# Kernel tuning notes

Measured on AMD Instinct MI355X. Metric: run time of the kernel, lower is better.

Reference implementation:

```python
import jax, jax.numpy as jnp
import numpy as np

SUB_NO = 20
T_NO = 201
E_NO = 2000
I_NO = 500
T_DATA = 20000

def _make_cden():
    C = np.zeros((SUB_NO, SUB_NO), dtype=np.float32)
    for i in range(SUB_NO):
        for c in (2 * i + 1, 2 * i + 2):
            if c < SUB_NO:
                C[i, c] = 1.0
    return C

C_DEN = _make_cden()
CHILDREN = [np.where(C_DEN[s] == 1)[0] for s in range(SUB_NO)]  # static tree structure


def setup_inputs() -> dict:
    key = jax.random.key(0)
    ks = jax.random.split(key, 12)
    eps = 1e-6
    inp = {}
    inp['S_e'] = jax.random.uniform(ks[0], (T_DATA, E_NO), dtype=jnp.float32)
    inp['S_i'] = jax.random.uniform(ks[1], (T_DATA, I_NO), dtype=jnp.float32)
    # uniform noise for REBAR reparam; clipped away from {0,1} so log(-log(u)) is finite
    inp['u'] = jnp.clip(jax.random.uniform(ks[2], (SUB_NO, E_NO + I_NO), dtype=jnp.float32), eps, 1.0 - eps)
    inp['v'] = jnp.clip(jax.random.uniform(ks[3], (SUB_NO, E_NO + I_NO), dtype=jnp.float32), eps, 1.0 - eps)
    inp['W_syn'] = jax.random.normal(ks[4], (SUB_NO, 2), dtype=jnp.float32) * 0.1
    inp['Tau_syn'] = jnp.ones((SUB_NO, 2), dtype=jnp.float32)
    inp['Delta_syn'] = jax.random.uniform(ks[5], (SUB_NO, 2), dtype=jnp.float32)
    inp['W_sub'] = jax.random.uniform(ks[6], (SUB_NO,), dtype=jnp.float32)
    inp['V_o'] = jax.random.normal(ks[7], (1,), dtype=jnp.float32)
    inp['Theta'] = jnp.zeros((SUB_NO,), dtype=jnp.float32)
    inp['C_syn_log'] = jnp.ones((SUB_NO, E_NO + I_NO), dtype=jnp.float32)
    return inp


def _H(x):
    # one-hot of per-column argmax (first max, as torch.argmax)
    idx = jnp.argmax(x, axis=0)
    return jax.nn.one_hot(idx, x.shape[0], axis=0, dtype=x.dtype)


def _reparam_pz(u, theta):
    return jnp.log(theta) - jnp.log(-jnp.log(u))


def _reparam_pz_b(v, b, theta):
    # b is one-hot per column; v_k = v at the b==1 row of each column
    v_k = jnp.sum(v * b, axis=0, keepdims=True)  # [1, cols]
    z_same = -jnp.log(-jnp.log(v))
    z_diff = -jnp.log(-jnp.log(v) / theta - jnp.log(v_k))
    return b * z_same + (1.0 - b) * z_diff


def _evaluate_f(C_syn, S_e, S_i, W_syn, Tau_syn, Delta_syn, W_sub, V_o):
    T_data = S_e.shape[0]
    C_syn_e = C_syn[:, :E_NO]          # [sub, E]
    C_syn_i = C_syn[:, -I_NO:]         # [sub, I]
    # double-exponential (alpha) synaptic kernels, vectorized over subunits & e/i
    t_raw = jnp.arange(T_NO, dtype=S_e.dtype)                               # [T_no]
    t = jnp.maximum(t_raw[None, None, :] - jnp.exp(Delta_syn)[:, :, None], 0.0)  # [sub,2,T_no]
    t_tau = t / jnp.exp(Tau_syn)[:, :, None]
    kern = t_tau * jnp.exp(-t_tau) * W_syn[:, :, None]                      # [sub,2,T_no]
    # project spikes onto subunits
    in_e = S_e @ C_syn_e.T   # [T, sub]
    in_i = S_i @ C_syn_i.T   # [T, sub]
    # causal depthwise conv: syn[t,s] = sum_tau kern[s,:,tau] * in[t-tau,s]
    inp = jnp.stack([in_e.T, in_i.T], axis=1).reshape(1, SUB_NO * 2, T_data)   # NCH
    k = jnp.flip(kern, axis=-1).reshape(SUB_NO * 2, 1, T_NO)                   # OIH
    filt = jax.lax.conv_general_dilated(
        inp, k, window_strides=(1,), padding=[(T_NO - 1, 0)],
        feature_group_count=SUB_NO * 2,
        dimension_numbers=('NCH', 'OIH', 'NCH'))
    syn_in = filt.reshape(SUB_NO, 2, T_data).sum(axis=1).T   # [T, sub]
    # tree-recurrent tanh aggregation (children have higher index than parents)
    sub_out = [None] * SUB_NO
    for s in range(SUB_NO):
        idx = SUB_NO - 1 - s
        ch = CHILDREN[idx]
        if ch.size == 0:
            sub_out[idx] = jnp.tanh(syn_in[:, idx])
        else:
            leaf = sum(sub_out[c] * W_sub[c] for c in ch)
            sub_out[idx] = jnp.tanh(syn_in[:, idx] + leaf)
    return sub_out[0] * W_sub[0] + V_o[0]


def reference(S_e, S_i, u, v, W_syn, Tau_syn, Delta_syn, W_sub, V_o, Theta, C_syn_log):
    theta = jax.nn.softmax(C_syn_log, axis=0)
    rebar_z = _reparam_pz(u, theta)
    hard_z = _H(rebar_z)
    rebar_zb = _reparam_pz_b(v, hard_z, theta)
    soft_z = jax.nn.sigmoid(rebar_z / 0.5) + 1e-9
    soft_zb = jax.nn.sigmoid(rebar_zb / 0.5) + 1e-9
    V_hard_z = _evaluate_f(hard_z, S_e, S_i, W_syn, Tau_syn, Delta_syn, W_sub, V_o)
    V_soft_z = _evaluate_f(soft_z, S_e, S_i, W_syn, Tau_syn, Delta_syn, W_sub, V_o)
    V_soft_zb = _evaluate_f(soft_zb, S_e, S_i, W_syn, Tau_syn, Delta_syn, W_sub, V_o)
    return (V_hard_z, V_soft_z, V_soft_zb, theta, hard_z, soft_z, soft_zb)
```

## Files before the change

### kernel.cpp

```cpp
#include <hip/hip_runtime.h>
#include <math.h>

#define SUBS 20
#define TAPS 201
#define ENO 2000
#define INO 500
#define TDATA 20000

typedef __bf16 bf16x8 __attribute__((ext_vector_type(8)));
typedef float f32x4 __attribute__((ext_vector_type(4)));

#define WGE_STRIDE 2048
#define WGI_STRIDE 512

#define WGE_OFF  0ull
#define WGI_OFF  262144ull
#define KERN_OFF 327680ull
#define INE_OFF  360448ull
#define INI_OFF  (INE_OFF + 4800000ull)
#define SYN_OFF  (INI_OFF + 4800000ull)

__device__ __forceinline__ unsigned short f2bf(float f) {
  union { float f; unsigned int u; } c; c.f = f;
  unsigned int u = c.u;
  return (unsigned short)((u + 0x7FFFu + ((u >> 16) & 1u)) >> 16);
}

__global__ __launch_bounds__(256) void prep_kernel(
    const float* __restrict__ u, const float* __restrict__ v,
    const float* __restrict__ C_log, const float* __restrict__ W_syn,
    const float* __restrict__ Tau_syn, const float* __restrict__ Delta_syn,
    float* __restrict__ out,
    unsigned short* __restrict__ wge, unsigned short* __restrict__ wgi,
    float* __restrict__ kern)
{
  if (blockIdx.x < 10) {
    const int n = blockIdx.x * 256 + threadIdx.x;
    if (n >= 2500) return;
    float x[SUBS], theta[SUBS], rebar[SUBS];
    float mx = -1e30f;
#pragma unroll
    for (int s = 0; s < SUBS; ++s) { x[s] = C_log[s*2500 + n]; mx = fmaxf(mx, x[s]); }
    float sum = 0.f;
#pragma unroll
    for (int s = 0; s < SUBS; ++s) { theta[s] = expf(x[s] - mx); sum += theta[s]; }
    const float inv = 1.f / sum;
    int idx = 0; float best = -1e30f;
#pragma unroll
    for (int s = 0; s < SUBS; ++s) {
      theta[s] *= inv;
      out[60000 + s*2500 + n] = theta[s];
      const float uu = u[s*2500 + n];
      const float r = logf(theta[s]) - logf(-logf(uu));
      rebar[s] = r;
      if (r > best) { best = r; idx = s; }
    }
    const float lvk = logf(v[idx*2500 + n]);
#pragma unroll
    for (int s = 0; s < SUBS; ++s) {
      const float hz = (s == idx) ? 1.f : 0.f;
      const float sz = 1.f / (1.f + expf(-2.f * rebar[s])) + 1e-9f;
      const float vv = v[s*2500 + n];
      const float zb = (s == idx) ? (-logf(-logf(vv)))
                                  : (-logf(-logf(vv) / theta[s] - lvk));
      const float szb = 1.f / (1.f + expf(-2.f * zb)) + 1e-9f;
      out[110000 + s*2500 + n] = hz;
      out[160000 + s*2500 + n] = sz;
      out[210000 + s*2500 + n] = szb;
      if (n < ENO) {
        wge[(s     )*WGE_STRIDE + n] = f2bf(hz);
        wge[(20 + s)*WGE_STRIDE + n] = f2bf(sz);
        wge[(40 + s)*WGE_STRIDE + n] = f2bf(szb);
      } else {
        const int k = n - ENO;
        wgi[(s     )*WGI_STRIDE + k] = f2bf(hz);
        wgi[(20 + s)*WGI_STRIDE + k] = f2bf(sz);
        wgi[(40 + s)*WGI_STRIDE + k] = f2bf(szb);
      }
    }
  } else {
    const int tid = threadIdx.x;
    for (int i = tid; i < 40*TAPS; i += 256) {
      const int ch = i / TAPS, m = i - ch*TAPS;
      const float dl  = expf(Delta_syn[ch]);
      const float tau = expf(Tau_syn[ch]);
      const float t  = fmaxf((float)m - dl, 0.f);
      const float tt = t / tau;
      kern[i] = tt * expf(-tt) * W_syn[ch];
    }
    for (int i = tid; i < 4*2048; i += 256) wge[(60 + (i >> 11))*WGE_STRIDE + (i & 2047)] = 0;
    for (int i = tid; i < 60*48;  i += 256) wge[(i / 48)*WGE_STRIDE + 2000 + (i % 48)] = 0;
    for (int i = tid; i < 4*512;  i += 256) wgi[(60 + (i >> 9))*WGI_STRIDE + (i & 511)] = 0;
    for (int i = tid; i < 60*12;  i += 256) wgi[(i / 12)*WGI_STRIDE + 500 + (i % 12)] = 0;
  }
}

__global__ __launch_bounds__(256) void gemm_kernel(
    const float* __restrict__ S_e, const float* __restrict__ S_i,
    const unsigned short* __restrict__ wge, const unsigned short* __restrict__ wgi,
    float* __restrict__ in_e, float* __restrict__ in_i, float* __restrict__ part)
{
  __shared__ unsigned short Alds[64*40];
  __shared__ unsigned short Blds[64*40];
  const int tid  = threadIdx.x;
  const int t0   = blockIdx.x * 64;
  const int chunk = blockIdx.y;
  const bool isE = (chunk < 2);
  const int wave = tid >> 6;
  const int lane = tid & 63;
  const int m16  = lane & 15;
  const int quad = lane >> 4;
  const int slotA = tid & 7;
  const int rowA  = tid >> 3;
  const int cB    = tid >> 2;
  const int slotB = tid & 3;

  const float* S = isE ? S_e : S_i;
  const unsigned short* Wg = isE ? wge : wgi;
  float* outp = (chunk == 0) ? in_e : ((chunk == 1) ? part : in_i);
  const int K       = isE ? ENO : INO;
  const int Wstride = isE ? WGE_STRIDE : WGI_STRIDE;
  const int k_base  = (chunk == 1) ? 1024 : 0;
  const int steps   = (chunk == 0) ? 32 : ((chunk == 1) ? 31 : 16);

  f32x4 acc0 = {0.f,0.f,0.f,0.f};
  f32x4 acc1 = acc0, acc2 = acc0, acc3 = acc0;

  for (int st = 0; st < steps; ++st) {
    const int k0 = k_base + st * 32;
#pragma unroll
    for (int p = 0; p < 2; ++p) {
      const int r = rowA + p*32;
      const int t = t0 + r;
      const int k = k0 + slotA*4;
      float4 val = make_float4(0.f, 0.f, 0.f, 0.f);
      if (t < TDATA) {
        if (k + 4 <= K) {
          val = *(const float4*)(S + (size_t)t*K + k);
        } else {
          val.x = (k+0 < K) ? S[(size_t)t*K + k+0] : 0.f;
          val.y = (k+1 < K) ? S[(size_t)t*K + k+1] : 0.f;
          val.z = (k+2 < K) ? S[(size_t)t*K + k+2] : 0.f;
          val.w = (k+3 < K) ? S[(size_t)t*K + k+3] : 0.f;
        }
      }
      ushort4 w4;
      w4.x = f2bf(val.x); w4.y = f2bf(val.y);
      w4.z = f2bf(val.z); w4.w = f2bf(val.w);
      *(ushort4*)(&Alds[r*40 + slotA*4]) = w4;
    }
    *(uint4*)(&Blds[cB*40 + slotB*8]) =
        *(const uint4*)(Wg + (size_t)cB*Wstride + k0 + slotB*8);
    __syncthreads();
    const bf16x8 a  = *(const bf16x8*)(&Alds[(wave*16 + m16)*40 + quad*8]);
    const bf16x8 b0 = *(const bf16x8*)(&Blds[(      m16)*40 + quad*8]);
    const bf16x8 b1 = *(const bf16x8*)(&Blds[(16 + m16)*40 + quad*8]);
    const bf16x8 b2 = *(const bf16x8*)(&Blds[(32 + m16)*40 + quad*8]);
    const bf16x8 b3 = *(const bf16x8*)(&Blds[(48 + m16)*40 + quad*8]);
    acc0 = __builtin_amdgcn_mfma_f32_16x16x32_bf16(a, b0, acc0, 0, 0, 0);
    acc1 = __builtin_amdgcn_mfma_f32_16x16x32_bf16(a, b1, acc1, 0, 0, 0);
    acc2 = __builtin_amdgcn_mfma_f32_16x16x32_bf16(a, b2, acc2, 0, 0, 0);
    acc3 = __builtin_amdgcn_mfma_f32_16x16x32_bf16(a, b3, acc3, 0, 0, 0);
    __syncthreads();
  }
  const int t = t0 + wave*16 + quad*4;
  if (t < TDATA) {
    float* o = outp + t;
    *(float4*)(o + (size_t)(     m16)*TDATA) = *(float4*)&acc0;
    *(float4*)(o + (size_t)(16 + m16)*TDATA) = *(float4*)&acc1;
    *(float4*)(o + (size_t)(32 + m16)*TDATA) = *(float4*)&acc2;
    if (m16 < 12)
      *(float4*)(o + (size_t)(48 + m16)*TDATA) = *(float4*)&acc3;
  }
}

__global__ __launch_bounds__(256) void reduce_kernel(
    float* __restrict__ in_e, const float* __restrict__ part)
{
  const int i = blockIdx.x * 256 + threadIdx.x;
  const int n4 = 60 * TDATA / 4;
  if (i < n4) {
    float4 a = ((const float4*)in_e)[i];
    const float4 p = ((const float4*)part)[i];
    a.x += p.x; a.y += p.y; a.z += p.z; a.w += p.w;
    ((float4*)in_e)[i] = a;
  }
}

__device__ __forceinline__ int swz(int i) { return i + (i >> 5); }

__global__ __launch_bounds__(256) void conv_kernel(
    const float* __restrict__ in_e, const float* __restrict__ in_i,
    const float* __restrict__ kern, float* __restrict__ syn)
{
  __shared__ float Ee[2320];
  __shared__ float Ei[2320];
  const int ch = blockIdx.y;
  const int t0 = blockIdx.x * 2048;
  const int s  = ch % SUBS;
  const float* pe = in_e + (size_t)ch * TDATA;
  const float* pi = in_i + (size_t)ch * TDATA;
  for (int i = threadIdx.x; i < 2248; i += 256) {
    const int g = t0 - 200 + i;
    const bool ok = (g >= 0) && (g < TDATA);
    Ee[swz(i)] = ok ? pe[g] : 0.f;
    Ei[swz(i)] = ok ? pi[g] : 0.f;
  }
  __syncthreads();
  const float* ke = kern + (size_t)(s*2    ) * TAPS;
  const float* ki = kern + (size_t)(s*2 + 1) * TAPS;
  const int tb = threadIdx.x * 8;
  float acc[8] = {0.f,0.f,0.f,0.f,0.f,0.f,0.f,0.f};
  float we[8], wi[8];
#pragma unroll
  for (int j = 0; j < 8; ++j) {
    we[j] = Ee[swz(tb + 200 + j)];
    wi[j] = Ei[swz(tb + 200 + j)];
  }
#pragma unroll 8
  for (int m = 0; m < TAPS; ++m) {
    const float k0 = ke[m];
    const float k1 = ki[m];
#pragma unroll
    for (int j = 0; j < 8; ++j)
      acc[j] = fmaf(we[j], k0, fmaf(wi[j], k1, acc[j]));
    if (m < TAPS - 1) {
#pragma unroll
      for (int j = 7; j > 0; --j) { we[j] = we[j-1]; wi[j] = wi[j-1]; }
      we[0] = Ee[swz(tb + 199 - m)];
      wi[0] = Ei[swz(tb + 199 - m)];
    }
  }
  const int t = t0 + tb;
  if (t < TDATA) {
    float* o = syn + (size_t)ch * TDATA + t;
    *(float4*)(o    ) = make_float4(acc[0], acc[1], acc[2], acc[3]);
    *(float4*)(o + 4) = make_float4(acc[4], acc[5], acc[6], acc[7]);
  }
}

__global__ __launch_bounds__(256) void tree_kernel(
    const float* __restrict__ syn, const float* __restrict__ W_sub,
    const float* __restrict__ V_o, float* __restrict__ out)
{
  const int t = blockIdx.x * 256 + threadIdx.x;
  const int var = blockIdx.y;
  if (t >= TDATA) return;
  const float* sp = syn + (size_t)var * SUBS * TDATA + t;
  float so[SUBS];
#pragma unroll
  for (int s = SUBS - 1; s >= 0; --s) {
    float val = sp[(size_t)s * TDATA];
    const int c1 = 2*s + 1, c2 = 2*s + 2;
    if (c1 < SUBS) val += so[c1] * W_sub[c1];
    if (c2 < SUBS) val += so[c2] * W_sub[c2];
    so[s] = tanhf(val);
  }
  out[(size_t)var * TDATA + t] = so[0] * W_sub[0] + V_o[0];
}

extern "C" void kernel_launch(void* const* d_in, const int* in_sizes, int n_in,
                              void* d_out, int out_size, void* d_ws, size_t ws_size,
                              hipStream_t stream) {
  const float* S_e     = (const float*)d_in[0];
  const float* S_i     = (const float*)d_in[1];
  const float* u       = (const float*)d_in[2];
  const float* v       = (const float*)d_in[3];
  const float* W_syn   = (const float*)d_in[4];
  const float* Tau_syn = (const float*)d_in[5];
  const float* Delta   = (const float*)d_in[6];
  const float* W_sub   = (const float*)d_in[7];
  const float* V_o     = (const float*)d_in[8];
  const float* C_log   = (const float*)d_in[10];
  float* out = (float*)d_out;
  char* ws = (char*)d_ws;
  unsigned short* wge = (unsigned short*)(ws + WGE_OFF);
  unsigned short* wgi = (unsigned short*)(ws + WGI_OFF);
  float* kern = (float*)(ws + KERN_OFF);
  float* in_e = (float*)(ws + INE_OFF);
  float* in_i = (float*)(ws + INI_OFF);
  float* syn  = (float*)(ws + SYN_OFF);

  prep_kernel<<<dim3(11), dim3(256), 0, stream>>>(u, v, C_log, W_syn, Tau_syn,
                                                  Delta, out, wge, wgi, kern);
  gemm_kernel<<<dim3(313, 3), dim3(256), 0, stream>>>(S_e, S_i, wge, wgi,
                                                      in_e, in_i, syn);
  reduce_kernel<<<dim3(1172), dim3(256), 0, stream>>>(in_e, syn);
  conv_kernel<<<dim3(10, 60), dim3(256), 0, stream>>>(in_e, in_i, kern, syn);
  tree_kernel<<<dim3(79, 3), dim3(256), 0, stream>>>(syn, W_sub, V_o, out);
}
```

Baseline: 343.6 us.

## Load GEMM operands straight to registers with prefetch and drop split-K reduce

The GEMM no longer stages operands in LDS. Each wave loads its own 16 rows of S and the bf16 weight fragments directly into registers, converts A to bf16 in registers, and prefetches the next K step while the current MFMAs run, so there are no block barriers. The split of the excitatory K range across two blocks, and the separate reduce kernel that summed the partial outputs, are removed. This saves a launch and a full read-modify-write pass over the 60x20000 intermediate. The costs are half as many blocks for the excitatory GEMM, which lowers parallelism on the bandwidth-bound S_e read, and redundant per-wave B loads served from cache. Tail reads are clamped to in-bounds addresses, and the zero-padded weights cancel the duplicated values.

Result: slower. 398.1 us (+15.9%).

```diff
diff --git a/kernel.cpp b/kernel.cpp
--- a/kernel.cpp
+++ b/kernel.cpp
@@ -9,6 +9,7 @@
 
 typedef __bf16 bf16x8 __attribute__((ext_vector_type(8)));
 typedef float f32x4 __attribute__((ext_vector_type(4)));
+typedef unsigned short ushort8 __attribute__((ext_vector_type(8)));
 
 #define WGE_STRIDE 2048
 #define WGI_STRIDE 512
@@ -98,93 +99,74 @@
 __global__ __launch_bounds__(256) void gemm_kernel(
     const float* __restrict__ S_e, const float* __restrict__ S_i,
     const unsigned short* __restrict__ wge, const unsigned short* __restrict__ wgi,
-    float* __restrict__ in_e, float* __restrict__ in_i, float* __restrict__ part)
-{
-  __shared__ unsigned short Alds[64*40];
-  __shared__ unsigned short Blds[64*40];
+    float* __restrict__ in_e, float* __restrict__ in_i)
+{
   const int tid  = threadIdx.x;
-  const int t0   = blockIdx.x * 64;
-  const int chunk = blockIdx.y;
-  const bool isE = (chunk < 2);
   const int wave = tid >> 6;
   const int lane = tid & 63;
   const int m16  = lane & 15;
   const int quad = lane >> 4;
-  const int slotA = tid & 7;
-  const int rowA  = tid >> 3;
-  const int cB    = tid >> 2;
-  const int slotB = tid & 3;
-
+  const int kq   = quad * 8;
+  const int t0   = blockIdx.x * 64 + wave * 16;
+  if (t0 >= TDATA) return;
+
+  const bool isE = (blockIdx.y == 0);
   const float* S = isE ? S_e : S_i;
   const unsigned short* Wg = isE ? wge : wgi;
-  float* outp = (chunk == 0) ? in_e : ((chunk == 1) ? part : in_i);
+  float* outp = isE ? in_e : in_i;
   const int K       = isE ? ENO : INO;
   const int Wstride = isE ? WGE_STRIDE : WGI_STRIDE;
-  const int k_base  = (chunk == 1) ? 1024 : 0;
-  const int steps   = (chunk == 0) ? 32 : ((chunk == 1) ? 31 : 16);
+  const int steps   = isE ? 63 : 16;
+
+  const float* Arow = S + (size_t)(t0 + m16) * K;
+  const unsigned short* Bp0 = Wg + (size_t)(     m16) * Wstride + kq;
+  const unsigned short* Bp1 = Wg + (size_t)(16 + m16) * Wstride + kq;
+  const unsigned short* Bp2 = Wg + (size_t)(32 + m16) * Wstride + kq;
+  const unsigned short* Bp3 = Wg + (size_t)(48 + m16) * Wstride + kq;
 
   f32x4 acc0 = {0.f,0.f,0.f,0.f};
   f32x4 acc1 = acc0, acc2 = acc0, acc3 = acc0;
 
+  auto ldA = [&](int k0, float4& lo, float4& hi) {
+    const int kb  = k0 + kq;
+    const int blo = (kb + 4 <= K) ? kb     : K - 4;
+    const int bhi = (kb + 8 <= K) ? kb + 4 : K - 4;
+    lo = *(const float4*)(Arow + blo);
+    hi = *(const float4*)(Arow + bhi);
+  };
+
+  float4 alo, ahi;
+  uint4 b0, b1, b2, b3;
+  ldA(0, alo, ahi);
+  b0 = *(const uint4*)(Bp0); b1 = *(const uint4*)(Bp1);
+  b2 = *(const uint4*)(Bp2); b3 = *(const uint4*)(Bp3);
+
   for (int st = 0; st < steps; ++st) {
-    const int k0 = k_base + st * 32;
-#pragma unroll
-    for (int p = 0; p < 2; ++p) {
-      const int r = rowA + p*32;
-      const int t = t0 + r;
-      const int k = k0 + slotA*4;
-      float4 val = make_float4(0.f, 0.f, 0.f, 0.f);
-      if (t < TDATA) {
-        if (k + 4 <= K) {
-          val = *(const float4*)(S + (size_t)t*K + k);
-        } else {
-          val.x = (k+0 < K) ? S[(size_t)t*K + k+0] : 0.f;
-          val.y = (k+1 < K) ? S[(size_t)t*K + k+1] : 0.f;
-          val.z = (k+2 < K) ? S[(size_t)t*K + k+2] : 0.f;
-          val.w = (k+3 < K) ? S[(size_t)t*K + k+3] : 0.f;
-        }
-      }
-      ushort4 w4;
-      w4.x = f2bf(val.x); w4.y = f2bf(val.y);
-      w4.z = f2bf(val.z); w4.w = f2bf(val.w);
-      *(ushort4*)(&Alds[r*40 + slotA*4]) = w4;
-    }
-    *(uint4*)(&Blds[cB*40 + slotB*8]) =
-        *(const uint4*)(Wg + (size_t)cB*Wstride + k0 + slotB*8);
-    __syncthreads();
-    const bf16x8 a  = *(const bf16x8*)(&Alds[(wave*16 + m16)*40 + quad*8]);
-    const bf16x8 b0 = *(const bf16x8*)(&Blds[(      m16)*40 + quad*8]);
-    const bf16x8 b1 = *(const bf16x8*)(&Blds[(16 + m16)*40 + quad*8]);
-    const bf16x8 b2 = *(const bf16x8*)(&Blds[(32 + m16)*40 + quad*8]);
-    const bf16x8 b3 = *(const bf16x8*)(&Blds[(48 + m16)*40 + quad*8]);
-    acc0 = __builtin_amdgcn_mfma_f32_16x16x32_bf16(a, b0, acc0, 0, 0, 0);
-    acc1 = __builtin_amdgcn_mfma_f32_16x16x32_bf16(a, b1, acc1, 0, 0, 0);
-    acc2 = __builtin_amdgcn_mfma_f32_16x16x32_bf16(a, b2, acc2, 0, 0, 0);
-    acc3 = __builtin_amdgcn_mfma_f32_16x16x32_bf16(a, b3, acc3, 0, 0, 0);
-    __syncthreads();
-  }
-  const int t = t0 + wave*16 + quad*4;
-  if (t < TDATA) {
-    float* o = outp + t;
-    *(float4*)(o + (size_t)(     m16)*TDATA) = *(float4*)&acc0;
-    *(float4*)(o + (size_t)(16 + m16)*TDATA) = *(float4*)&acc1;
-    *(float4*)(o + (size_t)(32 + m16)*TDATA) = *(float4*)&acc2;
-    if (m16 < 12)
-      *(float4*)(o + (size_t)(48 + m16)*TDATA) = *(float4*)&acc3;
-  }
-}
-
-__global__ __launch_bounds__(256) void reduce_kernel(
-    float* __restrict__ in_e, const float* __restrict__ part)
-{
-  const int i = blockIdx.x * 256 + threadIdx.x;
-  const int n4 = 60 * TDATA / 4;
-  if (i < n4) {
-    float4 a = ((const float4*)in_e)[i];
-    const float4 p = ((const float4*)part)[i];
-    a.x += p.x; a.y += p.y; a.z += p.z; a.w += p.w;
-    ((float4*)in_e)[i] = a;
-  }
+    const int kn = (st + 1 < steps) ? (st + 1) * 32 : st * 32;
+    float4 nalo, nahi;
+    ldA(kn, nalo, nahi);
+    const uint4 nb0 = *(const uint4*)(Bp0 + kn);
+    const uint4 nb1 = *(const uint4*)(Bp1 + kn);
+    const uint4 nb2 = *(const uint4*)(Bp2 + kn);
+    const uint4 nb3 = *(const uint4*)(Bp3 + kn);
+
+    ushort8 ap;
+    ap[0] = f2bf(alo.x); ap[1] = f2bf(alo.y); ap[2] = f2bf(alo.z); ap[3] = f2bf(alo.w);
+    ap[4] = f2bf(ahi.x); ap[5] = f2bf(ahi.y); ap[6] = f2bf(ahi.z); ap[7] = f2bf(ahi.w);
+    const bf16x8 af = *(const bf16x8*)&ap;
+    acc0 = __builtin_amdgcn_mfma_f32_16x16x32_bf16(af, *(const bf16x8*)&b0, acc0, 0, 0, 0);
+    acc1 = __builtin_amdgcn_mfma_f32_16x16x32_bf16(af, *(const bf16x8*)&b1, acc1, 0, 0, 0);
+    acc2 = __builtin_amdgcn_mfma_f32_16x16x32_bf16(af, *(const bf16x8*)&b2, acc2, 0, 0, 0);
+    acc3 = __builtin_amdgcn_mfma_f32_16x16x32_bf16(af, *(const bf16x8*)&b3, acc3, 0, 0, 0);
+    alo = nalo; ahi = nahi; b0 = nb0; b1 = nb1; b2 = nb2; b3 = nb3;
+  }
+
+  float* o = outp + t0 + quad * 4;
+  *(float4*)(o + (size_t)(     m16) * TDATA) = *(float4*)&acc0;
+  *(float4*)(o + (size_t)(16 + m16) * TDATA) = *(float4*)&acc1;
+  *(float4*)(o + (size_t)(32 + m16) * TDATA) = *(float4*)&acc2;
+  if (m16 < 12)
+    *(float4*)(o + (size_t)(48 + m16) * TDATA) = *(float4*)&acc3;
 }
 
 __device__ __forceinline__ int swz(int i) { return i + (i >> 5); }
@@ -283,9 +265,7 @@
 
   prep_kernel<<<dim3(11), dim3(256), 0, stream>>>(u, v, C_log, W_syn, Tau_syn,
                                                   Delta, out, wge, wgi, kern);
-  gemm_kernel<<<dim3(313, 3), dim3(256), 0, stream>>>(S_e, S_i, wge, wgi,
-                                                      in_e, in_i, syn);
-  reduce_kernel<<<dim3(1172), dim3(256), 0, stream>>>(in_e, syn);
+  gemm_kernel<<<dim3(313, 2), dim3(256), 0, stream>>>(S_e, S_i, wge, wgi, in_e, in_i);
   conv_kernel<<<dim3(10, 60), dim3(256), 0, stream>>>(in_e, in_i, kern, syn);
   tree_kernel<<<dim3(79, 3), dim3(256), 0, stream>>>(syn, W_sub, V_o, out);
 }
```

## Enlarge GEMM tiles to 128x64 and split K four ways with partial buffers

Applied to the files above, without the earlier changes.

The bf16 MFMA GEMM now uses 512-thread blocks covering 128 time rows with a K tile of 64, issuing two MFMA k-steps per barrier pair. K is split into four chunks for the excitatory input and two for the inhibitory input, giving six grid columns. Out-of-range A columns are clamped instead of branched, relying on the zero-padded weights to cancel them. Each chunk writes its own partial buffer, and the reduce kernel sums them, which adds extra workspace and more partial-sum memory traffic in exchange for more parallelism and fewer barriers per unit of work.

New measurement: 345.5 us. No clear change (+0.6%).

```diff
diff --git a/kernel.cpp b/kernel.cpp
--- a/kernel.cpp
+++ b/kernel.cpp
@@ -19,6 +19,9 @@
 #define INE_OFF  360448ull
 #define INI_OFF  (INE_OFF + 4800000ull)
 #define SYN_OFF  (INI_OFF + 4800000ull)
+#define P2_OFF   (SYN_OFF + 4800000ull)
+#define P3_OFF   (P2_OFF  + 4800000ull)
+#define P4_OFF   (P3_OFF  + 4800000ull)
 
 __device__ __forceinline__ unsigned short f2bf(float f) {
   union { float f; unsigned int u; } c; c.f = f;
@@ -95,72 +98,82 @@
   }
 }
 
-__global__ __launch_bounds__(256) void gemm_kernel(
+__global__ __launch_bounds__(512) void gemm_kernel(
     const float* __restrict__ S_e, const float* __restrict__ S_i,
     const unsigned short* __restrict__ wge, const unsigned short* __restrict__ wgi,
-    float* __restrict__ in_e, float* __restrict__ in_i, float* __restrict__ part)
-{
-  __shared__ unsigned short Alds[64*40];
-  __shared__ unsigned short Blds[64*40];
+    float* __restrict__ in_e, float* __restrict__ in_i,
+    float* __restrict__ P1, float* __restrict__ P2,
+    float* __restrict__ P3, float* __restrict__ P4)
+{
+  __shared__ unsigned short Alds[128*72];
+  __shared__ unsigned short Blds[64*72];
   const int tid  = threadIdx.x;
-  const int t0   = blockIdx.x * 64;
-  const int chunk = blockIdx.y;
-  const bool isE = (chunk < 2);
   const int wave = tid >> 6;
   const int lane = tid & 63;
   const int m16  = lane & 15;
   const int quad = lane >> 4;
-  const int slotA = tid & 7;
-  const int rowA  = tid >> 3;
-  const int cB    = tid >> 2;
-  const int slotB = tid & 3;
+  const int t0   = blockIdx.x * 128;
+  const int cy   = blockIdx.y;
+  const bool isE = (cy < 4);
 
   const float* S = isE ? S_e : S_i;
   const unsigned short* Wg = isE ? wge : wgi;
-  float* outp = (chunk == 0) ? in_e : ((chunk == 1) ? part : in_i);
+  float* outp = (cy == 0) ? in_e : (cy == 1) ? P1 : (cy == 2) ? P2
+              : (cy == 3) ? P3   : (cy == 4) ? in_i : P4;
   const int K       = isE ? ENO : INO;
   const int Wstride = isE ? WGE_STRIDE : WGI_STRIDE;
-  const int k_base  = (chunk == 1) ? 1024 : 0;
-  const int steps   = (chunk == 0) ? 32 : ((chunk == 1) ? 31 : 16);
+  const int k_base  = isE ? cy * 512 : (cy - 4) * 256;
+  const int steps   = isE ? 8 : 4;
+
+  const int rowA  = tid >> 2;
+  const int slotA = tid & 3;
+  const int rowB  = tid >> 3;
+  const int slotB = tid & 7;
+  const int tA    = t0 + rowA;
+  const float* Arow = S + (size_t)((tA < TDATA) ? tA : TDATA - 1) * K;
+  const unsigned short* Brow = Wg + (size_t)rowB * Wstride;
 
   f32x4 acc0 = {0.f,0.f,0.f,0.f};
   f32x4 acc1 = acc0, acc2 = acc0, acc3 = acc0;
 
   for (int st = 0; st < steps; ++st) {
-    const int k0 = k_base + st * 32;
-#pragma unroll
-    for (int p = 0; p < 2; ++p) {
-      const int r = rowA + p*32;
-      const int t = t0 + r;
-      const int k = k0 + slotA*4;
-      float4 val = make_float4(0.f, 0.f, 0.f, 0.f);
-      if (t < TDATA) {
-        if (k + 4 <= K) {
-          val = *(const float4*)(S + (size_t)t*K + k);
-        } else {
-          val.x = (k+0 < K) ? S[(size_t)t*K + k+0] : 0.f;
-          val.y = (k+1 < K) ? S[(size_t)t*K + k+1] : 0.f;
-          val.z = (k+2 < K) ? S[(size_t)t*K + k+2] : 0.f;
-          val.w = (k+3 < K) ? S[(size_t)t*K + k+3] : 0.f;
-        }
-      }
-      ushort4 w4;
-      w4.x = f2bf(val.x); w4.y = f2bf(val.y);
-      w4.z = f2bf(val.z); w4.w = f2bf(val.w);
-      *(ushort4*)(&Alds[r*40 + slotA*4]) = w4;
-    }
-    *(uint4*)(&Blds[cB*40 + slotB*8]) =
-        *(const uint4*)(Wg + (size_t)cB*Wstride + k0 + slotB*8);
+    const int k0 = k_base + st * 64;
+    const uint4 bw = *(const uint4*)(Brow + k0 + slotB*8);
+    float4 v0, v1, v2, v3;
+    {
+      const int kb = k0 + slotA*16;
+      const int c0 = (kb +  4 <= K) ? kb      : K - 4;
+      const int c1 = (kb +  8 <= K) ? kb +  4 : K - 4;
+      const int c2 = (kb + 12 <= K) ? kb +  8 : K - 4;
+      const int c3 = (kb + 16 <= K) ? kb + 12 : K - 4;
+      v0 = *(const float4*)(Arow + c0);
+      v1 = *(const float4*)(Arow + c1);
+      v2 = *(const float4*)(Arow + c2);
+      v3 = *(const float4*)(Arow + c3);
+    }
+    ushort4 p0, p1, p2, p3;
+    p0.x = f2bf(v0.x); p0.y = f2bf(v0.y); p0.z = f2bf(v0.z); p0.w = f2bf(v0.w);
+    p1.x = f2bf(v1.x); p1.y = f2bf(v1.y); p1.z = f2bf(v1.z); p1.w = f2bf(v1.w);
+    p2.x = f2bf(v2.x); p2.y = f2bf(v2.y); p2.z = f2bf(v2.z); p2.w = f2bf(v2.w);
+    p3.x = f2bf(v3.x); p3.y = f2bf(v3.y); p3.z = f2bf(v3.z); p3.w = f2bf(v3.w);
+    unsigned short* adst = &Alds[rowA*72 + slotA*16];
+    *(ushort4*)(adst    ) = p0;  *(ushort4*)(adst + 4) = p1;
+    *(ushort4*)(adst + 8) = p2;  *(ushort4*)(adst +12) = p3;
+    *(uint4*)(&Blds[rowB*72 + slotB*8]) = bw;
     __syncthreads();
-    const bf16x8 a  = *(const bf16x8*)(&Alds[(wave*16 + m16)*40 + quad*8]);
-    const bf16x8 b0 = *(const bf16x8*)(&Blds[(      m16)*40 + quad*8]);
-    const bf16x8 b1 = *(const bf16x8*)(&Blds[(16 + m16)*40 + quad*8]);
-    const bf16x8 b2 = *(const bf16x8*)(&Blds[(32 + m16)*40 + quad*8]);
-    const bf16x8 b3 = *(const bf16x8*)(&Blds[(48 + m16)*40 + quad*8]);
-    acc0 = __builtin_amdgcn_mfma_f32_16x16x32_bf16(a, b0, acc0, 0, 0, 0);
-    acc1 = __builtin_amdgcn_mfma_f32_16x16x32_bf16(a, b1, acc1, 0, 0, 0);
-    acc2 = __builtin_amdgcn_mfma_f32_16x16x32_bf16(a, b2, acc2, 0, 0, 0);
-    acc3 = __builtin_amdgcn_mfma_f32_16x16x32_bf16(a, b3, acc3, 0, 0, 0);
+#pragma unroll
+    for (int h = 0; h < 2; ++h) {
+      const int kh = h*32 + quad*8;
+      const bf16x8 a  = *(const bf16x8*)(&Alds[(wave*16 + m16)*72 + kh]);
+      const bf16x8 b0 = *(const bf16x8*)(&Blds[(      m16)*72 + kh]);
+      const bf16x8 b1 = *(const bf16x8*)(&Blds[(16 + m16)*72 + kh]);
+      const bf16x8 b2 = *(const bf16x8*)(&Blds[(32 + m16)*72 + kh]);
+      const bf16x8 b3 = *(const bf16x8*)(&Blds[(48 + m16)*72 + kh]);
+      acc0 = __builtin_amdgcn_mfma_f32_16x16x32_bf16(a, b0, acc0, 0, 0, 0);
+      acc1 = __builtin_amdgcn_mfma_f32_16x16x32_bf16(a, b1, acc1, 0, 0, 0);
+      acc2 = __builtin_amdgcn_mfma_f32_16x16x32_bf16(a, b2, acc2, 0, 0, 0);
+      acc3 = __builtin_amdgcn_mfma_f32_16x16x32_bf16(a, b3, acc3, 0, 0, 0);
+    }
     __syncthreads();
   }
   const int t = t0 + wave*16 + quad*4;
@@ -175,14 +188,29 @@
 }
 
 __global__ __launch_bounds__(256) void reduce_kernel(
-    float* __restrict__ in_e, const float* __restrict__ part)
-{
+    float* __restrict__ in_e, float* __restrict__ in_i,
+    const float* __restrict__ P1, const float* __restrict__ P2,
+    const float* __restrict__ P3, const float* __restrict__ P4)
+{
+  const int n4 = 60 * TDATA / 4;
+  if (blockIdx.x >= 1172) {
+    const int i = (blockIdx.x - 1172) * 256 + threadIdx.x;
+    if (i < n4) {
+      float4 a = ((const float4*)in_i)[i];
+      const float4 p = ((const float4*)P4)[i];
+      a.x += p.x; a.y += p.y; a.z += p.z; a.w += p.w;
+      ((float4*)in_i)[i] = a;
+    }
+    return;
+  }
   const int i = blockIdx.x * 256 + threadIdx.x;
-  const int n4 = 60 * TDATA / 4;
   if (i < n4) {
     float4 a = ((const float4*)in_e)[i];
-    const float4 p = ((const float4*)part)[i];
-    a.x += p.x; a.y += p.y; a.z += p.z; a.w += p.w;
+    const float4 p1 = ((const float4*)P1)[i];
+    const float4 p2 = ((const float4*)P2)[i];
+    const float4 p3 = ((const float4*)P3)[i];
+    a.x += p1.x + p2.x + p3.x; a.y += p1.y + p2.y + p3.y;
+    a.z += p1.z + p2.z + p3.z; a.w += p1.w + p2.w + p3.w;
     ((float4*)in_e)[i] = a;
   }
 }
@@ -280,12 +308,16 @@
   float* in_e = (float*)(ws + INE_OFF);
   float* in_i = (float*)(ws + INI_OFF);
   float* syn  = (float*)(ws + SYN_OFF);
+  float* P1   = syn;
+  float* P2   = (float*)(ws + P2_OFF);
+  float* P3   = (float*)(ws + P3_OFF);
+  float* P4   = (float*)(ws + P4_OFF);
 
   prep_kernel<<<dim3(11), dim3(256), 0, stream>>>(u, v, C_log, W_syn, Tau_syn,
                                                   Delta, out, wge, wgi, kern);
-  gemm_kernel<<<dim3(313, 3), dim3(256), 0, stream>>>(S_e, S_i, wge, wgi,
-                                                      in_e, in_i, syn);
-  reduce_kernel<<<dim3(1172), dim3(256), 0, stream>>>(in_e, syn);
+  gemm_kernel<<<dim3(157, 6), dim3(512), 0, stream>>>(
+      S_e, S_i, wge, wgi, in_e, in_i, P1, P2, P3, P4);
+  reduce_kernel<<<dim3(2344), dim3(256), 0, stream>>>(in_e, in_i, P1, P2, P3, P4);
   conv_kernel<<<dim3(10, 60), dim3(256), 0, stream>>>(in_e, in_i, kern, syn);
   tree_kernel<<<dim3(79, 3), dim3(256), 0, stream>>>(syn, W_sub, V_o, out);
 }
```
